# Kernel tuning notes

Hardware: AMD Instinct MI355X
Metric: run time of the kernel (lower is better)

Reference implementation:

```python
import jax, jax.numpy as jnp
import numpy as np
from jax import lax


def get_grid(h, w):
    # normalized [-1,1] grid, channel 0 = x, channel 1 = y, shape [1,h,w,2]
    gx, gy = jnp.meshgrid(jnp.linspace(-1.0, 1.0, w), jnp.linspace(-1.0, 1.0, h))
    return jnp.stack([gx, gy], axis=-1)[None].astype(jnp.float32)


def gaussian_kernel(k, sigma=1.0):
    c = jnp.arange(k, dtype=jnp.float32) - (k - 1) / 2.0
    g = jnp.exp(-(c ** 2) / (2.0 * sigma ** 2))
    k2 = jnp.outer(g, g)
    return k2 / k2.sum()


def resize_bilinear(x, H, W):
    # x: [B,C,h,w]; torch F.interpolate(mode='bilinear', align_corners=False)
    B, C, h, w = x.shape
    def coords(n_out, n_in):
        c = (jnp.arange(n_out, dtype=jnp.float32) + 0.5) * (n_in / n_out) - 0.5
        c = jnp.clip(c, 0.0, n_in - 1.0)
        lo = jnp.floor(c).astype(jnp.int32)
        hi = jnp.minimum(lo + 1, n_in - 1)
        return lo, hi, c - lo.astype(jnp.float32)
    y0, y1, wy = coords(H, h)
    x0, x1, wx = coords(W, w)
    r = x[:, :, y0, :] * (1.0 - wy)[None, None, :, None] + x[:, :, y1, :] * wy[None, None, :, None]
    return r[:, :, :, x0] * (1.0 - wx) + r[:, :, :, x1] * wx


def _forward(src_grid, kernel, src_grid_base, tgt_grid, niter):
    B = src_grid.shape[0]
    H, W = tgt_grid.shape[1], tgt_grid.shape[2]
    ks = kernel.shape[-1]
    HW = H * W
    # forward displacement, resampled to target resolution, in pixel units
    dsrc = (src_grid - src_grid_base).transpose(0, 3, 1, 2)        # [B,2,Hs,Ws]
    dsrc = resize_bilinear(dsrc, H, W)                              # [B,2,H,W]
    dx = dsrc[:, 0].reshape(B, HW) * (W / 2.0)
    dy = dsrc[:, 1].reshape(B, HW) * (H / 2.0)
    xg = (jnp.arange(HW) % W).astype(jnp.float32)
    yg = (jnp.arange(HW) // W).astype(jnp.float32)
    xi = jnp.round(xg[None] + dx).astype(jnp.int32)
    yi = jnp.round(yg[None] + dy).astype(jnp.int32)
    oob = (xi < 0) | (yi < 0) | (xi > W - 1) | (yi > H - 1)
    field = jnp.where(oob, -1, yi * W + xi) + 1   # index 0 = trash slot
    # sort + dedup: duplicates are redirected to the trash slot
    order = jnp.argsort(field, axis=1)            # stable
    sf = jnp.take_along_axis(field, order, axis=1)
    keep = jnp.concatenate([jnp.ones((B, 1), bool), sf[:, 1:] != sf[:, :-1]], axis=1)
    sf = sf * keep
    inv_order = jnp.argsort(order, axis=1)
    field = jnp.take_along_axis(sf, inv_order, axis=1)
    # scatter inverse displacement (unique indices except trash slot 0)
    z = jnp.zeros((B, 1), dtype=dx.dtype)
    dxp = jnp.concatenate([z, dx], axis=1)
    dyp = jnp.concatenate([z, dy], axis=1)
    fieldp = jnp.concatenate([jnp.zeros((B, 1), field.dtype), field], axis=1)
    bidx = jnp.arange(B)[:, None]
    inv_dx = jnp.zeros_like(dxp).at[bidx, fieldp].set(-dxp)[:, 1:].reshape(B, H, W)
    inv_dy = jnp.zeros_like(dyp).at[bidx, fieldp].set(-dyp)[:, 1:].reshape(B, H, W)
    mask = (jnp.zeros_like(dxp).at[bidx, fieldp].set(1.0)[:, 1:].reshape(B, H, W)) > 0.5
    # pad so hole-fill never reads outside
    p = niter + 1
    inv_dx = jnp.pad(inv_dx, ((0, 0), (p, p), (p, p)))
    inv_dy = jnp.pad(inv_dy, ((0, 0), (p, p), (p, p)))
    mask = jnp.pad(mask, ((0, 0), (p, p), (p, p)))
    pd = ks // 2
    k4 = kernel.reshape(1, 1, ks, ks)
    def conv(x):
        return lax.conv_general_dilated(x[:, None], k4, (1, 1), [(pd, pd), (pd, pd)])[:, 0]
    # hole-fill: dilate mask by 4-neighborhood, fill with gaussian-weighted avg
    for _ in range(niter):
        nb = (jnp.pad(mask, ((0, 0), (1, 0), (0, 0)))[:, :-1]
              | jnp.pad(mask, ((0, 0), (0, 1), (0, 0)))[:, 1:]
              | jnp.pad(mask, ((0, 0), (0, 0), (1, 0)))[:, :, :-1]
              | jnp.pad(mask, ((0, 0), (0, 0), (0, 1)))[:, :, 1:])
        new_mask = (~mask) & nb
        new_dx = conv(inv_dx)
        new_dy = conv(inv_dy)
        new_sum = conv(mask.astype(inv_dx.dtype))
        denom = jnp.where(new_mask, new_sum, 1.0)  # safe: new_sum>0 where new_mask
        inv_dx = jnp.where(new_mask, new_dx / denom, inv_dx)
        inv_dy = jnp.where(new_mask, new_dy / denom, inv_dy)
        mask = mask | new_mask
    # erode: drop pixels with any unmasked 4-neighbor (outside counts as masked)
    for _ in range(niter):
        full = (jnp.pad(mask, ((0, 0), (1, 0), (0, 0)), constant_values=True)[:, :-1]
                & jnp.pad(mask, ((0, 0), (0, 1), (0, 0)), constant_values=True)[:, 1:]
                & jnp.pad(mask, ((0, 0), (0, 0), (1, 0)), constant_values=True)[:, :, :-1]
                & jnp.pad(mask, ((0, 0), (0, 0), (0, 1)), constant_values=True)[:, :, 1:])
        mask = mask & full
    inv_dx = jnp.where(mask, inv_dx, 2.0 * W)
    inv_dy = jnp.where(mask, inv_dy, 2.0 * H)
    inv_dx = inv_dx[:, p:-p, p:-p]
    inv_dy = inv_dy[:, p:-p, p:-p]
    dtgt = jnp.stack([inv_dx * (2.0 / W), inv_dy * (2.0 / H)], axis=3)
    return tgt_grid + dtgt


def setup_inputs() -> dict:
    key = jax.random.key(0)
    B, Hs, Ws, H, W = 8, 256, 256, 512, 512
    base = get_grid(Hs, Ws)
    src_grid = base + 0.05 * jax.random.normal(key, (B, Hs, Ws, 2), jnp.float32)
    return {
        "src_grid": src_grid,
        "kernel": gaussian_kernel(3),
        "src_grid_base": base,
        "tgt_grid": get_grid(H, W),
        "niter": 5,
    }


def reference(src_grid, kernel, src_grid_base, tgt_grid, niter):
    return _forward(src_grid, kernel, src_grid_base, tgt_grid, niter)
```

## Files before the change

### kernel.cpp

```cpp
#include <hip/hip_runtime.h>
#include <hip/hip_fp16.h>

typedef unsigned long long u64;
typedef unsigned int u32;
typedef float float4a __attribute__((ext_vector_type(4), aligned(4)));

#define B_    8
#define HS_   256
#define WS_   256
#define H_    512
#define W_    512
#define HW_   (H_ * W_)
#define TO_Y  16
#define NTILE 32
#define WR    36
#define WCOLS 276
#define WSTR  277
#define NBAND 32
#define NBKT  64
#define INFW  0xFFFFFFFFu
#define CAPB  8192

__device__ __forceinline__ void bilin_disp(const float* __restrict__ src,
                                           const float* __restrict__ base,
                                           int b, int y, int x,
                                           float& dx, float& dy) {
#pragma clang fp contract(off)
    float cy = ((float)y + 0.5f) * 0.5f - 0.5f;
    cy = fminf(fmaxf(cy, 0.0f), 255.0f);
    int   y0 = (int)floorf(cy);
    int   y1 = min(y0 + 1, HS_ - 1);
    float wy = cy - (float)y0;

    float cx = ((float)x + 0.5f) * 0.5f - 0.5f;
    cx = fminf(fmaxf(cx, 0.0f), 255.0f);
    int   x0 = (int)floorf(cx);
    float wx = cx - (float)x0;

    float omy = 1.0f - wy;
    float wA, wB;
    int xs;
    if (x0 >= WS_ - 1) { xs = WS_ - 2; wA = 0.0f; wB = 1.0f; }
    else               { xs = x0;      wA = 1.0f - wx; wB = wx; }

    const float4a* S0 = (const float4a*)(src  + ((b * HS_ + y0) * WS_ + xs) * 2);
    const float4a* S1 = (const float4a*)(src  + ((b * HS_ + y1) * WS_ + xs) * 2);
    const float4a* B0 = (const float4a*)(base + (y0 * WS_ + xs) * 2);
    const float4a* B1 = (const float4a*)(base + (y1 * WS_ + xs) * 2);
    float4a s0 = *S0, s1 = *S1, b0 = *B0, b1 = *B1;

    float a00x = s0.x - b0.x, a00y = s0.y - b0.y;
    float a01x = s0.z - b0.z, a01y = s0.w - b0.w;
    float a10x = s1.x - b1.x, a10y = s1.y - b1.y;
    float a11x = s1.z - b1.z, a11y = s1.w - b1.w;

    float r0x = a00x * omy + a10x * wy;
    float r0y = a00y * omy + a10y * wy;
    float r1x = a01x * omy + a11x * wy;
    float r1y = a01y * omy + a11y * wy;
    dx = (r0x * wA + r1x * wB) * 256.0f;
    dy = (r0y * wA + r1y * wB) * 256.0f;
}

__device__ __forceinline__ u32 pack16(float x, float y) {
    __half hx = __float2half_rn(x), hy = __float2half_rn(y);
    return ((u32)__half_as_ushort(hy) << 16) | (u32)__half_as_ushort(hx);
}
__device__ __forceinline__ float2 unpack16(u32 p) {
    float2 f;
    f.x = __half2float(__ushort_as_half((unsigned short)(p & 0xFFFFu)));
    f.y = __half2float(__ushort_as_half((unsigned short)(p >> 16)));
    return f;
}

__device__ __forceinline__ u64 shfl_left(u64 v) {
    unsigned lo = __shfl_up((unsigned)v, 1);
    unsigned hi = __shfl_up((unsigned)(v >> 32), 1);
    u64 r = ((u64)hi << 32) | lo;
    return (threadIdx.x & 63) ? r : 0ull;
}
__device__ __forceinline__ u64 shfl_right(u64 v) {
    unsigned lo = __shfl_down((unsigned)v, 1);
    unsigned hi = __shfl_down((unsigned)(v >> 32), 1);
    u64 r = ((u64)hi << 32) | lo;
    return ((threadIdx.x & 63) == 63) ? 0ull : r;
}

__launch_bounds__(1024)
__global__ void pre_k(const float* __restrict__ src,
                      const float* __restrict__ base,
                      u32* __restrict__ pay,
                      u32* __restrict__ gcount,
                      u32* __restrict__ bucket) {
    __shared__ u32 cnt[NBKT];
    __shared__ u32 bbase[NBKT];

    int bid = blockIdx.x;
    int b   = bid & 7;
    int t   = bid >> 3;
    int j   = t * 1024 + threadIdx.x;
    int y   = j >> 9;
    int x   = j & (W_ - 1);

    if (threadIdx.x < NBKT) cnt[threadIdx.x] = 0;
    __syncthreads();

    float dx, dy;
    bilin_disp(src, base, b, y, x, dx, dy);
    pay[b * HW_ + j] = pack16(-dx, -dy);

    int xi = (int)rintf((float)x + dx);
    int yi = (int)rintf((float)y + dy);
    bool inb = (xi >= 0 && xi < W_ && yi >= 0 && yi < H_);
    int bk0 = 0, bk1 = -1;
    u32 r0 = 0, r1 = 0, e = 0;
    if (inb) {
        int band = yi >> 4;
        bk0 = band * 2 + (xi >> 8);
        r0 = atomicAdd(&cnt[bk0], 1u);
        if      (xi >= 246 && xi <= 255) bk1 = band * 2 + 1;
        else if (xi >= 256 && xi <= 265) bk1 = band * 2;
        if (bk1 >= 0) r1 = atomicAdd(&cnt[bk1], 1u);
        e = ((u32)(yi & 15) << 27) | ((u32)xi << 18) | (u32)j;
    }
    __syncthreads();
    if (threadIdx.x < NBKT) {
        u32 c = cnt[threadIdx.x];
        bbase[threadIdx.x] = c ? atomicAdd(&gcount[b * NBKT + threadIdx.x], c)
                               : 0u;
    }
    __syncthreads();
    if (inb) {
        u32 s0 = bbase[bk0] + r0;
        if (s0 < CAPB) bucket[(b * NBKT + bk0) * CAPB + s0] = e;
        if (bk1 >= 0) {
            u32 s1 = bbase[bk1] + r1;
            if (s1 < CAPB) bucket[(b * NBKT + bk1) * CAPB + s1] = e;
        }
    }
}

__launch_bounds__(512, 2)
__global__ void fused5_k(const u32* __restrict__ pay,
                         const u32* __restrict__ gcount,
                         const u32* __restrict__ bucket,
                         const float* __restrict__ kern,
                         const float* __restrict__ tgt,
                         float* __restrict__ out) {
    __shared__ u32 plane[WR * WSTR];

    int id   = blockIdx.x;
    int b    = id & 7;
    int rest = id >> 3;
    int tile = rest >> 1;
    int half = rest & 1;
    int X0   = half << 8;
    int Y0   = tile * TO_Y;
    int w0   = Y0 - 10;
    int wc0  = X0 - 10;
    int tid  = threadIdx.x;

    float kw[9];
#pragma unroll
    for (int q = 0; q < 9; q++) kw[q] = kern[q];

    for (int i = tid; i < WR * WSTR; i += 512) plane[i] = INFW;
    __syncthreads();

    {
        int qlo = max(0, w0 >> 4);
        int qhi = min(NBAND - 1, (w0 + WR - 1) >> 4);
        for (int q = qlo; q <= qhi; q++) {
            int bki = b * NBKT + q * 2 + half;
            u32 cntq = min(gcount[bki], (u32)CAPB);
            const u32* bk = bucket + bki * CAPB;
            int ybase = q * 16 - w0;
            for (u32 i = tid; i < cntq; i += 512) {
                u32 e  = bk[i];
                int wr = ybase + (int)((e >> 27) & 15u);
                if ((unsigned)wr < WR) {
                    int xc = (int)((e >> 18) & 511u) - wc0;
                    atomicMin(&plane[wr * WSTR + xc], e & 0x3FFFFu);
                }
            }
        }
    }
    __syncthreads();

    int wv   = tid >> 6;
    int lane = tid & 63;
    int col  = X0 + 32 * wv - 16 + lane;
    int cls  = col - wc0;
    bool inwin = ((unsigned)cls < WCOLS);
    bool colin = inwin && (col >= -6) && (col <= W_ + 5);

    u64 m = 0;
    if (colin) {
#pragma unroll 6
        for (int r = 0; r < WR; r++)
            m |= (u64)(plane[r * WSTR + cls] != INFW) << r;
    }
    __syncthreads();

    {
        const u32* pb = pay + b * HW_;
        for (int idx = tid; idx < WR * WCOLS; idx += 512) {
            int rr = idx / WCOLS;
            int cc = idx - rr * WCOLS;
            int off = rr * WSTR + cc;
            u32 k = plane[off];
            plane[off] = (k != INFW) ? pb[k] : 0u;
        }
    }
    __syncthreads();

    int rlo = max(0, -6 - w0);
    int rhi = min(WR - 1, (W_ + 5) - w0);
    u64 validm = colin ? ((((u64)1 << (rhi - rlo + 1)) - 1) << rlo) : 0ull;

    const u64 VROWS = (((u64)1 << 24) - 1) << 6;
    bool vlane = (lane >= 6 && lane <= 57);

    for (int it = 0; it < 5; it++) {
        u64 mL = shfl_left(m), mR = shfl_right(m);
        u64 cand = ~m & ((m << 1) | (m >> 1) | mL | mR) & validm;
        u64 cv = vlane ? (cand & VROWS) : 0ull;
        while (cv) {
            int r = __builtin_ctzll(cv);
            cv &= cv - 1;
            float s = 0.0f, ax = 0.0f, ay = 0.0f;
#pragma unroll
            for (int dr = -1; dr <= 1; dr++) {
#pragma unroll
                for (int dc = -1; dc <= 1; dc++) {
                    if (dr == 0 && dc == 0) continue;
                    u64 nm = (dc < 0) ? mL : ((dc > 0) ? mR : m);
                    float wq = ((nm >> (r + dr)) & 1)
                                 ? kw[(dr + 1) * 3 + (dc + 1)] : 0.0f;
                    int cc = min(max(cls + dc, 0), WCOLS - 1);
                    float2 nv = unpack16(plane[(r + dr) * WSTR + cc]);
                    s += wq; ax += wq * nv.x; ay += wq * nv.y;
                }
            }
            float rs = __builtin_amdgcn_rcpf(s);
            plane[r * WSTR + cls] = pack16(ax * rs, ay * rs);
        }
        m |= cand;
        __syncthreads();
    }

    for (int it = 0; it < 5; it++) {
        u64 mL = shfl_left(m), mR = shfl_right(m);
        m &= (m << 1) & (m >> 1) & mL & mR;
    }

    if (lane >= 16 && lane < 48) {
#pragma unroll 4
        for (int r = 10; r < 10 + TO_Y; r++) {
            int row = w0 + r;
            bool on = (m >> r) & 1;
            float vx, vy;
            if (on) {
                float2 t = unpack16(plane[r * WSTR + cls]);
                vx = t.x * (1.0f / 256.0f);
                vy = t.y * (1.0f / 256.0f);
            } else {
                vx = 4.0f; vy = 4.0f;
            }
            int ti = (row * W_ + col) * 2;
            float2 tg = *(const float2*)(tgt + ti);
            float2 ov; ov.x = tg.x + vx; ov.y = tg.y + vy;
            ((float2*)out)[(size_t)b * HW_ + row * W_ + col] = ov;
        }
    }
}

extern "C" void kernel_launch(void* const* d_in, const int* in_sizes, int n_in,
                              void* d_out, int out_size, void* d_ws, size_t ws_size,
                              hipStream_t stream) {
    const float* src  = (const float*)d_in[0];
    const float* kern = (const float*)d_in[1];
    const float* base = (const float*)d_in[2];
    const float* tgt  = (const float*)d_in[3];
    float* out = (float*)d_out;

    char* ws = (char*)d_ws;
    u32* gcount = (u32*)ws;
    u32* pay    = (u32*)(ws + 4096);
    u32* bucket = (u32*)(ws + 4096 + (size_t)B_ * HW_ * 4);

    hipMemsetAsync(gcount, 0, B_ * NBKT * sizeof(u32), stream);

    pre_k<<<(B_ * HW_) / 1024, 1024, 0, stream>>>(src, base, pay, gcount, bucket);
    fused5_k<<<512, 512, 0, stream>>>(pay, gcount, bucket, kern, tgt, out);
}
```

Measured before the change: 136.9 us.

## Embed displacement payload in 64-bit bucket entries and aggregate bucket atomics per wave

The separate per-pixel payload array is dropped. The packed displacement now travels inside 64-bit bucket entries, and the shared-memory scatter uses a 64-bit atomicMin keyed on the source index in the high bits. This removes the payload write and the random global gather in the second kernel. In exchange the bucket traffic and the LDS plane double in size, since the plane becomes u64, which may limit occupancy. Bucket slot ranks are now taken with wave-level ballot aggregation instead of one shared atomic per thread.

```diff
diff --git a/kernel.cpp b/kernel.cpp
--- a/kernel.cpp
+++ b/kernel.cpp
@@ -12,7 +12,6 @@
 #define W_    512
 #define HW_   (H_ * W_)
 #define TO_Y  16
-#define NTILE 32
 #define WR    36
 #define WCOLS 276
 #define WSTR  277
@@ -89,65 +88,82 @@
 __launch_bounds__(1024)
 __global__ void pre_k(const float* __restrict__ src,
                       const float* __restrict__ base,
-                      u32* __restrict__ pay,
                       u32* __restrict__ gcount,
-                      u32* __restrict__ bucket) {
+                      u64* __restrict__ bucket) {
     __shared__ u32 cnt[NBKT];
     __shared__ u32 bbase[NBKT];
 
-    int bid = blockIdx.x;
-    int b   = bid & 7;
-    int t   = bid >> 3;
-    int j   = t * 1024 + threadIdx.x;
-    int y   = j >> 9;
-    int x   = j & (W_ - 1);
+    int bid  = blockIdx.x;
+    int b    = bid & 7;
+    int t    = bid >> 3;
+    int j    = t * 1024 + threadIdx.x;
+    int y    = j >> 9;
+    int x    = j & (W_ - 1);
+    int lane = threadIdx.x & 63;
+    u64 lmlt = ((u64)1 << lane) - 1;
 
     if (threadIdx.x < NBKT) cnt[threadIdx.x] = 0;
     __syncthreads();
 
     float dx, dy;
     bilin_disp(src, base, b, y, x, dx, dy);
-    pay[b * HW_ + j] = pack16(-dx, -dy);
 
     int xi = (int)rintf((float)x + dx);
     int yi = (int)rintf((float)y + dy);
     bool inb = (xi >= 0 && xi < W_ && yi >= 0 && yi < H_);
     int bk0 = 0, bk1 = -1;
-    u32 r0 = 0, r1 = 0, e = 0;
+    u32 rank0 = 0, rank1 = 0;
+    u64 e = 0;
     if (inb) {
         int band = yi >> 4;
         bk0 = band * 2 + (xi >> 8);
-        r0 = atomicAdd(&cnt[bk0], 1u);
         if      (xi >= 246 && xi <= 255) bk1 = band * 2 + 1;
         else if (xi >= 256 && xi <= 265) bk1 = band * 2;
-        if (bk1 >= 0) r1 = atomicAdd(&cnt[bk1], 1u);
-        e = ((u32)(yi & 15) << 27) | ((u32)xi << 18) | (u32)j;
-    }
-    __syncthreads();
+        e = ((u64)(u32)j << 46) | ((u64)(u32)(yi & 15) << 42)
+          | ((u64)(u32)xi << 33) | (u64)pack16(-dx, -dy);
+    }
+
+    u64 act = __ballot(inb);
+    while (act) {
+        int ldr = __builtin_ctzll(act);
+        int bq  = __shfl(bk0, ldr, 64);
+        u64 same = __ballot(inb && (bk0 == bq));
+        u32 basev = 0;
+        if (lane == ldr)
+            basev = atomicAdd(&cnt[bq], (u32)__builtin_popcountll(same));
+        basev = __shfl(basev, ldr, 64);
+        if (inb && bk0 == bq)
+            rank0 = basev + (u32)__builtin_popcountll(same & lmlt);
+        act &= ~same;
+    }
+    if (bk1 >= 0) rank1 = atomicAdd(&cnt[bk1], 1u);
+    __syncthreads();
+
     if (threadIdx.x < NBKT) {
         u32 c = cnt[threadIdx.x];
         bbase[threadIdx.x] = c ? atomicAdd(&gcount[b * NBKT + threadIdx.x], c)
                                : 0u;
     }
     __syncthreads();
+
     if (inb) {
-        u32 s0 = bbase[bk0] + r0;
+        u32 s0 = bbase[bk0] + rank0;
         if (s0 < CAPB) bucket[(b * NBKT + bk0) * CAPB + s0] = e;
         if (bk1 >= 0) {
-            u32 s1 = bbase[bk1] + r1;
+            u32 s1 = bbase[bk1] + rank1;
             if (s1 < CAPB) bucket[(b * NBKT + bk1) * CAPB + s1] = e;
         }
     }
 }
 
 __launch_bounds__(512, 2)
-__global__ void fused5_k(const u32* __restrict__ pay,
-                         const u32* __restrict__ gcount,
-                         const u32* __restrict__ bucket,
+__global__ void fused6_k(const u32* __restrict__ gcount,
+                         const u64* __restrict__ bucket,
                          const float* __restrict__ kern,
                          const float* __restrict__ tgt,
                          float* __restrict__ out) {
-    __shared__ u32 plane[WR * WSTR];
+    __shared__ u64 plane[WR * WSTR];
+    u32* vals = (u32*)plane;
 
     int id   = blockIdx.x;
     int b    = id & 7;
@@ -164,7 +180,7 @@
 #pragma unroll
     for (int q = 0; q < 9; q++) kw[q] = kern[q];
 
-    for (int i = tid; i < WR * WSTR; i += 512) plane[i] = INFW;
+    for (int i = tid; i < WR * WSTR; i += 512) plane[i] = ~0ull;
     __syncthreads();
 
     {
@@ -173,14 +189,14 @@
         for (int q = qlo; q <= qhi; q++) {
             int bki = b * NBKT + q * 2 + half;
             u32 cntq = min(gcount[bki], (u32)CAPB);
-            const u32* bk = bucket + bki * CAPB;
+            const u64* bk = bucket + (size_t)bki * CAPB;
             int ybase = q * 16 - w0;
             for (u32 i = tid; i < cntq; i += 512) {
-                u32 e  = bk[i];
-                int wr = ybase + (int)((e >> 27) & 15u);
+                u64 e  = bk[i];
+                int wr = ybase + (int)((e >> 42) & 15u);
                 if ((unsigned)wr < WR) {
-                    int xc = (int)((e >> 18) & 511u) - wc0;
-                    atomicMin(&plane[wr * WSTR + xc], e & 0x3FFFFu);
+                    int xc = (int)((e >> 33) & 511u) - wc0;
+                    atomicMin(&plane[wr * WSTR + xc], e);
                 }
             }
         }
@@ -198,18 +214,29 @@
     if (colin) {
 #pragma unroll 6
         for (int r = 0; r < WR; r++)
-            m |= (u64)(plane[r * WSTR + cls] != INFW) << r;
-    }
-    __syncthreads();
-
-    {
-        const u32* pb = pay + b * HW_;
-        for (int idx = tid; idx < WR * WCOLS; idx += 512) {
+            m |= (u64)(((const u32*)plane)[(r * WSTR + cls) * 2 + 1] != INFW) << r;
+    }
+
+    u32 regs[20];
+#pragma unroll
+    for (int k = 0; k < 20; k++) {
+        int idx = tid + k * 512;
+        if (idx < WR * WCOLS) {
             int rr = idx / WCOLS;
             int cc = idx - rr * WCOLS;
-            int off = rr * WSTR + cc;
-            u32 k = plane[off];
-            plane[off] = (k != INFW) ? pb[k] : 0u;
+            u64 v = plane[rr * WSTR + cc];
+            regs[k] = ((u32)(v >> 32) == INFW) ? 0u : (u32)v;
+        }
+    }
+    __syncthreads();
+
+#pragma unroll
+    for (int k = 0; k < 20; k++) {
+        int idx = tid + k * 512;
+        if (idx < WR * WCOLS) {
+            int rr = idx / WCOLS;
+            int cc = idx - rr * WCOLS;
+            vals[rr * WSTR + cc] = regs[k];
         }
     }
     __syncthreads();
@@ -238,12 +265,12 @@
                     float wq = ((nm >> (r + dr)) & 1)
                                  ? kw[(dr + 1) * 3 + (dc + 1)] : 0.0f;
                     int cc = min(max(cls + dc, 0), WCOLS - 1);
-                    float2 nv = unpack16(plane[(r + dr) * WSTR + cc]);
+                    float2 nv = unpack16(vals[(r + dr) * WSTR + cc]);
                     s += wq; ax += wq * nv.x; ay += wq * nv.y;
                 }
             }
             float rs = __builtin_amdgcn_rcpf(s);
-            plane[r * WSTR + cls] = pack16(ax * rs, ay * rs);
+            vals[r * WSTR + cls] = pack16(ax * rs, ay * rs);
         }
         m |= cand;
         __syncthreads();
@@ -261,7 +288,7 @@
             bool on = (m >> r) & 1;
             float vx, vy;
             if (on) {
-                float2 t = unpack16(plane[r * WSTR + cls]);
+                float2 t = unpack16(vals[r * WSTR + cls]);
                 vx = t.x * (1.0f / 256.0f);
                 vy = t.y * (1.0f / 256.0f);
             } else {
@@ -286,11 +313,10 @@
 
     char* ws = (char*)d_ws;
     u32* gcount = (u32*)ws;
-    u32* pay    = (u32*)(ws + 4096);
-    u32* bucket = (u32*)(ws + 4096 + (size_t)B_ * HW_ * 4);
+    u64* bucket = (u64*)(ws + 4096);
 
     hipMemsetAsync(gcount, 0, B_ * NBKT * sizeof(u32), stream);
 
-    pre_k<<<(B_ * HW_) / 1024, 1024, 0, stream>>>(src, base, pay, gcount, bucket);
-    fused5_k<<<512, 512, 0, stream>>>(pay, gcount, bucket, kern, tgt, out);
-}
+    pre_k<<<(B_ * HW_) / 1024, 1024, 0, stream>>>(src, base, gcount, bucket);
+    fused6_k<<<512, 512, 0, stream>>>(gcount, bucket, kern, tgt, out);
+}
```

Result: no change. 139.3 us (+1.8%).
